# Kernel tuning notes

Hardware: AMD Instinct MI355X
Metric: run time of the kernel (lower is better)

Reference implementation:

```python
import jax, jax.numpy as jnp
import numpy as np

B, C, T, F = 2, 256, 1024, 64
N, HID = 4, 64


def setup_inputs() -> dict:
    key = jax.random.key(0)
    ks = jax.random.split(key, 9)
    s = 0.02
    return {
        "x": jax.random.normal(ks[0], (B, C, T, F), dtype=jnp.float32),
        "Wq": jax.random.normal(ks[1], (N, HID, C), dtype=jnp.float32) * s,
        "bq": jnp.zeros((N, HID), dtype=jnp.float32),
        "Wk": jax.random.normal(ks[2], (N, HID, C), dtype=jnp.float32) * s,
        "bk": jnp.zeros((N, HID), dtype=jnp.float32),
        "Wv": jax.random.normal(ks[3], (N, C // N, C), dtype=jnp.float32) * s,
        "bv": jnp.zeros((N, C // N), dtype=jnp.float32),
        "Wp": jax.random.normal(ks[4], (C, C), dtype=jnp.float32) * s,
        "bp": jnp.zeros((C,), dtype=jnp.float32),
    }


def reference(x, Wq, bq, Wk, bk, Wv, bv, Wp, bp):
    b, c, t, f = x.shape
    n = Wq.shape[0]
    # conv1x1 per head then torch: cat(dim=0) -> [N*b, h, t, f]; transpose(1,2); flatten -> [N*b, t, h*f]
    def proj(W, bias):
        h = W.shape[1]
        y = jnp.einsum('bctf,nhc->nbthf', x, W) + bias[:, None, None, :, None]
        return y.reshape(n * b, t, h * f)

    Q = proj(Wq, bq)                       # [N*b, t, hid*f]
    K = proj(Wk, bk)                       # [N*b, t, hid*f]
    V = proj(Wv, bv)                       # [N*b, t, (c/N)*f]

    scale = 1.0 / jnp.sqrt(jnp.asarray(Q.shape[-1], dtype=x.dtype))
    attn = jax.nn.softmax(jnp.einsum('mte,mse->mts', Q, K) * scale, axis=2)
    Vo = jnp.einsum('mts,msd->mtd', attn, V)             # [N*b, t, c*f/N]

    # torch: reshape(b*N, t, c*f//N).transpose(1,2).view(N,b,c//N,t,f).transpose(0,1).view(b,c,t,f)
    Vo = Vo.transpose(0, 2, 1)                            # [N*b, c*f/N, t]
    Vo = Vo.reshape(n, b, c // n, t, f)
    Vo = jnp.swapaxes(Vo, 0, 1).reshape(b, c, t, f)

    out = jnp.einsum('bctf,oc->botf', Vo, Wp) + bp[None, :, None, None]
    return out + x
```

## Files before the change

kernel.cpp:

```cpp
#include <hip/hip_runtime.h>

#define DI __device__ __forceinline__

static constexpr int B_ = 2;
static constexpr int C_ = 256;
static constexpr int T_ = 1024;
static constexpr int F_ = 64;
static constexpr int M_ = 8;
static constexpr int E_ = 4096;
static constexpr float SCALE_ = 1.0f / 64.0f;

typedef __attribute__((ext_vector_type(8))) short bf16x8;
typedef __attribute__((ext_vector_type(4))) float f32x4;

DI unsigned short bf16_rne(float f) {
    unsigned int u = __float_as_uint(f);
    return (unsigned short)((u + 0x7FFFu + ((u >> 16) & 1u)) >> 16);
}
DI float bf2f(unsigned short h) { return __uint_as_float(((unsigned int)h) << 16); }
DI ushort4 pack4(float a, float b, float c, float d) {
    return make_ushort4(bf16_rne(a), bf16_rne(b), bf16_rne(c), bf16_rne(d));
}
DI float4 up4(ushort4 u) {
    return make_float4(bf2f(u.x), bf2f(u.y), bf2f(u.z), bf2f(u.w));
}

DI void gload_lds16(const unsigned short* g, unsigned short* l) {
    __builtin_amdgcn_global_load_lds(
        (const __attribute__((address_space(1))) unsigned int*)g,
        (__attribute__((address_space(3))) unsigned int*)l, 16, 0, 0);
}

DI void mfma16(f32x4& acc, bf16x8 a, bf16x8 b) {
    asm("v_mfma_f32_16x16x32_bf16 %0, %1, %2, %0" : "+v"(acc) : "v"(a), "v"(b));
}

__global__ __launch_bounds__(256) void wconv_kernel(
    const float* __restrict__ Wq, const float* __restrict__ Wk,
    const float* __restrict__ Wv, const float* __restrict__ Wp,
    const float* __restrict__ bq, const float* __restrict__ bk,
    const float* __restrict__ bv,
    unsigned short* __restrict__ Wall, unsigned short* __restrict__ Wpb,
    float* __restrict__ bias_all)
{
    const int tid = (int)threadIdx.x;
    const int bid = (int)blockIdx.x;
    if (bid < 192) {
        const int idx = (bid * 256 + tid) * 4;
        const int proj = idx >> 16, rem = idx & 65535;
        const float* src = proj == 0 ? Wq : (proj == 1 ? Wk : Wv);
        float4 v = *(const float4*)(src + rem);
        *(ushort4*)(Wall + idx) = pack4(v.x, v.y, v.z, v.w);
        const int gid = bid * 256 + tid;
        if (gid < 768) {
            float bb = gid < 256 ? bq[gid] : (gid < 512 ? bk[gid - 256] : bv[gid - 512]);
            bias_all[gid] = bb;
        }
    } else {
        const int idx = ((bid - 192) * 256 + tid) * 4;
        float4 v = *(const float4*)(Wp + idx);
        *(ushort4*)(Wpb + idx) = pack4(v.x, v.y, v.z, v.w);
    }
}

__global__ __launch_bounds__(256) void qkv_one(
    const float* __restrict__ x, const unsigned short* __restrict__ Wall,
    const float* __restrict__ bias_all, unsigned short* __restrict__ outQ)
{
    const int wgid = (int)blockIdx.x;
    const int b = wgid >> 9, tft = wgid & 511;
    const int tfbase = tft * 128;

    const int tid = (int)threadIdx.x;
    const int wid = tid >> 6, lane = tid & 63;
    const int wr = wid >> 1, wc = wid & 1;
    const int lo16 = lane & 15, hi4 = lane >> 4;

    __shared__ unsigned short As[4 * 128 * 64];
    __shared__ unsigned short Bs[128 * 64];

    {
        const int a = lane & 7, cg = lane >> 3;
        const int rowb = wid * 32 + a * 4;
        const float* xb = x + (size_t)b * (C_ * T_ * F_) + tfbase + rowb;
        for (int cb = 0; cb < 256; cb += 64) {
            const int c0 = cb + cg * 8;
            float4 v[8];
#pragma unroll
            for (int g = 0; g < 8; ++g)
                v[g] = *(const float4*)(xb + (size_t)(c0 + g) * 65536);
            const int kc = cb >> 6;
#pragma unroll
            for (int j = 0; j < 4; ++j) {
                const int row = rowb + j;
                const int col8 = cg ^ (row & 7);
                ushort4 lo = pack4(v[0].x + 0.f, v[1].x, v[2].x, v[3].x);
                float e0 = (&v[0].x)[j], e1 = (&v[1].x)[j], e2 = (&v[2].x)[j], e3 = (&v[3].x)[j];
                float e4 = (&v[4].x)[j], e5 = (&v[5].x)[j], e6 = (&v[6].x)[j], e7 = (&v[7].x)[j];
                ushort4 p0 = pack4(e0, e1, e2, e3);
                ushort4 p1 = pack4(e4, e5, e6, e7);
                (void)lo;
                *(ushort4*)&As[kc * 8192 + row * 64 + col8 * 8]     = p0;
                *(ushort4*)&As[kc * 8192 + row * 64 + col8 * 8 + 4] = p1;
            }
        }
    }

    const int srow = lane >> 3;
    const int scol = ((lane & 7) ^ srow) * 8;
    const int tf0 = tfbase + wr * 64;

    __syncthreads();

    for (int ntl = 0; ntl < 6; ++ntl) {
        const int nbase = ntl * 128;
        const unsigned short* brow = Wall + (size_t)nbase * 256;
        f32x4 acc[4][4] = {};

        for (int kc = 0; kc < 4; ++kc) {
#pragma unroll
            for (int i = 0; i < 4; ++i) {
                const int rb = wid * 32 + i * 8;
                gload_lds16(brow + (size_t)(rb + srow) * 256 + kc * 64 + scol,
                            &Bs[rb * 64]);
            }
            __syncthreads();
#pragma unroll
            for (int kk = 0; kk < 2; ++kk) {
                const int hc = (kk * 32 + hi4 * 8) ^ ((lane & 7) << 3);
                bf16x8 a[4], bb[4];
#pragma unroll
                for (int mi = 0; mi < 4; ++mi)
                    a[mi] = *(const bf16x8*)&As[kc * 8192 + (wr * 64 + mi * 16 + lo16) * 64 + hc];
#pragma unroll
                for (int nj = 0; nj < 4; ++nj)
                    bb[nj] = *(const bf16x8*)&Bs[(wc * 64 + nj * 16 + lo16) * 64 + hc];
#pragma unroll
                for (int mi = 0; mi < 4; ++mi)
#pragma unroll
                    for (int nj = 0; nj < 4; ++nj)
                        mfma16(acc[mi][nj], a[mi], bb[nj]);
            }
            __syncthreads();
        }

        asm volatile("s_nop 7\n\ts_nop 7" ::: "memory");
#pragma unroll
        for (int nj = 0; nj < 4; ++nj) {
            const int r_col = nbase + wc * 64 + nj * 16 + lo16;
            const int projl = r_col >> 8;
            const int rr = r_col & 255;
            const int mrow = (rr >> 6) * 2 + b;
            const int h = rr & 63;
            const float bv = bias_all[r_col];
            unsigned short* dst0 = outQ + (size_t)projl * 33554432
                                 + (size_t)mrow * (T_ * E_) + h * 64;
#pragma unroll
            for (int mi = 0; mi < 4; ++mi) {
                const int tf = tf0 + mi * 16 + hi4 * 4;
                const int t = tf >> 6, f = tf & 63;
                *(ushort4*)(dst0 + (size_t)t * E_ + f) =
                    pack4(acc[mi][nj][0] + bv, acc[mi][nj][1] + bv,
                          acc[mi][nj][2] + bv, acc[mi][nj][3] + bv);
            }
        }
        if (ntl < 5) __syncthreads();
    }
}

__global__ __launch_bounds__(256) void scores_mfma(
    const unsigned short* __restrict__ Q, const unsigned short* __restrict__ K,
    unsigned short* __restrict__ S)
{
    const int orig = (int)blockIdx.x;
    const int wg = (orig & 7) * 64 + (orig >> 3);
    const int m = wg >> 6;
    const int rest = wg & 63;
    const int sbase = (rest & 7) * 128;
    const int tbase = (rest >> 3) * 128;
    const int tid = (int)threadIdx.x;
    const int wid = tid >> 6, lane = tid & 63;
    const int wr = wid >> 1, wc = wid & 1;
    const int lo16 = lane & 15, hi4 = lane >> 4;

    __shared__ unsigned short As[128 * 64];
    __shared__ unsigned short Bs[128 * 64];

    f32x4 acc[4][4] = {};

    const unsigned short* qrow = Q + ((size_t)m * T_ + tbase) * E_;
    const unsigned short* krow = K + ((size_t)m * T_ + sbase) * E_;

    const int srow = lane >> 3;
    const int scol = ((lane & 7) ^ srow) * 8;

    for (int eb = 0; eb < E_; eb += 64) {
#pragma unroll
        for (int i = 0; i < 4; ++i) {
            const int rb = wid * 32 + i * 8;
            gload_lds16(qrow + (size_t)(rb + srow) * E_ + eb + scol, &As[rb * 64]);
            gload_lds16(krow + (size_t)(rb + srow) * E_ + eb + scol, &Bs[rb * 64]);
        }
        __syncthreads();
#pragma unroll
        for (int kk = 0; kk < 2; ++kk) {
            const int hc = (kk * 32 + hi4 * 8) ^ ((lane & 7) << 3);
            bf16x8 a[4], bb[4];
#pragma unroll
            for (int mi = 0; mi < 4; ++mi)
                a[mi] = *(const bf16x8*)&As[(wr * 64 + mi * 16 + lo16) * 64 + hc];
#pragma unroll
            for (int nj = 0; nj < 4; ++nj)
                bb[nj] = *(const bf16x8*)&Bs[(wc * 64 + nj * 16 + lo16) * 64 + hc];
#pragma unroll
            for (int mi = 0; mi < 4; ++mi)
#pragma unroll
                for (int nj = 0; nj < 4; ++nj)
                    mfma16(acc[mi][nj], a[mi], bb[nj]);
        }
        __syncthreads();
    }

    asm volatile("s_nop 7\n\ts_nop 7" ::: "memory");
#pragma unroll
    for (int mi = 0; mi < 4; ++mi)
#pragma unroll
        for (int r = 0; r < 4; ++r) {
            int trow = tbase + wr * 64 + mi * 16 + hi4 * 4 + r;
            unsigned short* sp = S + ((size_t)m * T_ + trow) * T_ + sbase + wc * 64 + lo16;
#pragma unroll
            for (int nj = 0; nj < 4; ++nj)
                sp[nj * 16] = bf16_rne(acc[mi][nj][r] * SCALE_);
        }
}

__global__ __launch_bounds__(256) void softmax_kernel(
    const unsigned short* __restrict__ S, unsigned short* __restrict__ A)
{
    const size_t rowoff = ((size_t)blockIdx.y * T_ + blockIdx.x) * T_;
    const int tid = (int)threadIdx.x;
    const int wid = tid >> 6, lane = tid & 63;

    __shared__ float redmx[4];
    __shared__ float redsm[4];

    float4 v = up4(*(const ushort4*)(S + rowoff + tid * 4));
    float mx = fmaxf(fmaxf(v.x, v.y), fmaxf(v.z, v.w));
#pragma unroll
    for (int off = 32; off > 0; off >>= 1) mx = fmaxf(mx, __shfl_xor(mx, off));
    if (lane == 0) redmx[wid] = mx;
    __syncthreads();
    mx = fmaxf(fmaxf(redmx[0], redmx[1]), fmaxf(redmx[2], redmx[3]));

    float e0 = __expf(v.x - mx), e1 = __expf(v.y - mx);
    float e2 = __expf(v.z - mx), e3 = __expf(v.w - mx);
    float sm = (e0 + e1) + (e2 + e3);
#pragma unroll
    for (int off = 32; off > 0; off >>= 1) sm += __shfl_xor(sm, off);
    if (lane == 0) redsm[wid] = sm;
    __syncthreads();
    sm = (redsm[0] + redsm[1]) + (redsm[2] + redsm[3]);
    float inv = 1.0f / sm;
    *(ushort4*)(A + rowoff + tid * 4) = pack4(e0 * inv, e1 * inv, e2 * inv, e3 * inv);
}

__global__ __launch_bounds__(256) void vt_kernel(
    const unsigned short* __restrict__ V, unsigned short* __restrict__ Vt)
{
    const int m = blockIdx.z;
    const int d0 = blockIdx.x * 64;
    const int s0 = blockIdx.y * 64;
    const int tid = (int)threadIdx.x;
    __shared__ unsigned short ts[64][68];

    const unsigned short* vp = V + (size_t)m * T_ * E_;
#pragma unroll
    for (int it = 0; it < 4; ++it) {
        int idx = it * 256 + tid;
        int sl = idx >> 4, d4 = (idx & 15) * 4;
        *(ushort4*)&ts[sl][d4] = *(const ushort4*)&vp[(size_t)(s0 + sl) * E_ + d0 + d4];
    }
    __syncthreads();
    unsigned short* op = Vt + (size_t)m * E_ * T_;
    const int dl = tid >> 2, s16 = (tid & 3) * 16;
#pragma unroll
    for (int q = 0; q < 4; ++q) {
        int s4 = s16 + q * 4;
        ushort4 v = make_ushort4(ts[s4][dl], ts[s4+1][dl], ts[s4+2][dl], ts[s4+3][dl]);
        *(ushort4*)&op[(size_t)(d0 + dl) * T_ + s0 + s4] = v;
    }
}

__global__ __launch_bounds__(256) void pv_mfma(
    const unsigned short* __restrict__ A, const unsigned short* __restrict__ Vt,
    unsigned short* __restrict__ G)
{
    const int orig = (int)blockIdx.x;
    const int wg = (orig & 7) * 256 + (orig >> 3);
    const int m = wg >> 8;
    const int rest = wg & 255;
    const int dbase = (rest & 31) * 128;
    const int tbase = (rest >> 5) * 128;
    const int nh = m >> 1, b = m & 1;
    const int tid = (int)threadIdx.x;
    const int wid = tid >> 6, lane = tid & 63;
    const int wr = wid >> 1, wc = wid & 1;
    const int lo16 = lane & 15, hi4 = lane >> 4;

    __shared__ unsigned short As[128 * 64];
    __shared__ unsigned short Bs[128 * 64];

    f32x4 acc[4][4] = {};

    const unsigned short* arow = A  + ((size_t)m * T_ + tbase) * T_;
    const unsigned short* vrow = Vt + (size_t)m * E_ * T_ + (size_t)dbase * T_;

    const int srow = lane >> 3;
    const int scol = ((lane & 7) ^ srow) * 8;

    for (int sb = 0; sb < T_; sb += 64) {
#pragma unroll
        for (int i = 0; i < 4; ++i) {
            const int rb = wid * 32 + i * 8;
            gload_lds16(arow + (size_t)(rb + srow) * T_ + sb + scol, &As[rb * 64]);
            gload_lds16(vrow + (size_t)(rb + srow) * T_ + sb + scol, &Bs[rb * 64]);
        }
        __syncthreads();
#pragma unroll
        for (int kk = 0; kk < 2; ++kk) {
            const int hc = (kk * 32 + hi4 * 8) ^ ((lane & 7) << 3);
            bf16x8 a[4], bb[4];
#pragma unroll
            for (int mi = 0; mi < 4; ++mi)
                a[mi] = *(const bf16x8*)&As[(wr * 64 + mi * 16 + lo16) * 64 + hc];
#pragma unroll
            for (int nj = 0; nj < 4; ++nj)
                bb[nj] = *(const bf16x8*)&Bs[(wc * 64 + nj * 16 + lo16) * 64 + hc];
#pragma unroll
            for (int mi = 0; mi < 4; ++mi)
#pragma unroll
                for (int nj = 0; nj < 4; ++nj)
                    mfma16(acc[mi][nj], a[mi], bb[nj]);
        }
        __syncthreads();
    }

    asm volatile("s_nop 7\n\ts_nop 7" ::: "memory");
    const int cb   = nh * 64 + (dbase >> 6) + wc;
    const int t2lo = (tbase >> 6) + wr;
#pragma unroll
    for (int mi = 0; mi < 4; ++mi) {
        const int tl = mi * 16 + hi4 * 4;
#pragma unroll
        for (int nj = 0; nj < 4; ++nj) {
            const int d63 = nj * 16 + lo16;
            size_t addr = (((size_t)(b * 256 + cb)) * 1024 + d63 * 16 + t2lo) * 64 + tl;
            *(ushort4*)&G[addr] = pack4(acc[mi][nj][0], acc[mi][nj][1],
                                        acc[mi][nj][2], acc[mi][nj][3]);
        }
    }
}

__global__ __launch_bounds__(256) void gt_kernel(
    const unsigned short* __restrict__ G, unsigned short* __restrict__ GT)
{
    const int tf0 = blockIdx.x * 64;
    const int c0  = blockIdx.y * 64;
    const int b   = blockIdx.z;
    const int tid = (int)threadIdx.x;
    __shared__ unsigned short ts[64][68];

    const unsigned short* gb = G + (size_t)(b * 256 + c0) * 65536 + tf0;
#pragma unroll
    for (int it = 0; it < 4; ++it) {
        int idx = it * 256 + tid;
        int cl = idx >> 4, tf4 = (idx & 15) * 4;
        *(ushort4*)&ts[cl][tf4] = *(const ushort4*)(gb + (size_t)cl * 65536 + tf4);
    }
    __syncthreads();
    const int tfl = tid >> 2, c16 = (tid & 3) * 16;
    unsigned short* op = GT + ((size_t)b * 65536 + tf0 + tfl) * 256 + c0 + c16;
#pragma unroll
    for (int q = 0; q < 4; ++q) {
        int cl = c16 + q * 4;
        ushort4 v = make_ushort4(ts[cl][tfl], ts[cl+1][tfl], ts[cl+2][tfl], ts[cl+3][tfl]);
        *(ushort4*)(op + q * 4) = v;
    }
}

__global__ __launch_bounds__(256) void outproj_mfma(
    const unsigned short* __restrict__ GT, const unsigned short* __restrict__ Wpb,
    const float* __restrict__ bp, const float* __restrict__ x,
    float* __restrict__ out)
{
    const int tfbase = blockIdx.x * 128;
    const int obase  = blockIdx.y * 128;
    const int b      = blockIdx.z;
    const int tid = (int)threadIdx.x;
    const int wid = tid >> 6, lane = tid & 63;
    const int wr = wid >> 1, wc = wid & 1;
    const int lo16 = lane & 15, hi4 = lane >> 4;

    __shared__ unsigned short As[128 * 64];
    __shared__ unsigned short Bs[128 * 64];

    f32x4 acc[4][4] = {};

    const unsigned short* arow = GT + ((size_t)b * 65536 + tfbase) * 256;
    const unsigned short* brow = Wpb + (size_t)obase * 256;

    const int srow = lane >> 3;
    const int scol = ((lane & 7) ^ srow) * 8;

    for (int cb = 0; cb < 256; cb += 64) {
#pragma unroll
        for (int i = 0; i < 4; ++i) {
            const int rb = wid * 32 + i * 8;
            gload_lds16(arow + (size_t)(rb + srow) * 256 + cb + scol, &As[rb * 64]);
            gload_lds16(brow + (size_t)(rb + srow) * 256 + cb + scol, &Bs[rb * 64]);
        }
        __syncthreads();
#pragma unroll
        for (int kk = 0; kk < 2; ++kk) {
            const int hc = (kk * 32 + hi4 * 8) ^ ((lane & 7) << 3);
            bf16x8 a[4], bb[4];
#pragma unroll
            for (int mi = 0; mi < 4; ++mi)
                a[mi] = *(const bf16x8*)&As[(wr * 64 + mi * 16 + lo16) * 64 + hc];
#pragma unroll
            for (int nj = 0; nj < 4; ++nj)
                bb[nj] = *(const bf16x8*)&Bs[(wc * 64 + nj * 16 + lo16) * 64 + hc];
#pragma unroll
            for (int mi = 0; mi < 4; ++mi)
#pragma unroll
                for (int nj = 0; nj < 4; ++nj)
                    mfma16(acc[mi][nj], a[mi], bb[nj]);
        }
        __syncthreads();
    }

    asm volatile("s_nop 7\n\ts_nop 7" ::: "memory");
#pragma unroll
    for (int nj = 0; nj < 4; ++nj) {
        const int o = obase + wc * 64 + nj * 16 + lo16;
        const float bias = bp[o];
        const size_t rowb = ((size_t)(b * 256 + o)) * 65536;
#pragma unroll
        for (int mi = 0; mi < 4; ++mi) {
            const int tf = tfbase + wr * 64 + mi * 16 + hi4 * 4;
            float4 xv = *(const float4*)(x + rowb + tf);
            float4 r = make_float4(acc[mi][nj][0] + bias + xv.x,
                                   acc[mi][nj][1] + bias + xv.y,
                                   acc[mi][nj][2] + bias + xv.z,
                                   acc[mi][nj][3] + bias + xv.w);
            *(float4*)(out + rowb + tf) = r;
        }
    }
}

extern "C" void kernel_launch(void* const* d_in, const int* in_sizes, int n_in,
                              void* d_out, int out_size, void* d_ws, size_t ws_size,
                              hipStream_t stream) {
    const float* x  = (const float*)d_in[0];
    const float* Wq = (const float*)d_in[1];
    const float* bq = (const float*)d_in[2];
    const float* Wk = (const float*)d_in[3];
    const float* bk = (const float*)d_in[4];
    const float* Wv = (const float*)d_in[5];
    const float* bv = (const float*)d_in[6];
    const float* Wp = (const float*)d_in[7];
    const float* bp = (const float*)d_in[8];
    float* out = (float*)d_out;

    char* ws = (char*)d_ws;
    unsigned short* Q    = (unsigned short*)(ws);
    unsigned short* K    = (unsigned short*)(ws + 67108864);
    unsigned short* V    = (unsigned short*)(ws + 134217728);
    unsigned short* S    = (unsigned short*)(ws + 201326592);
    unsigned short* A    = (unsigned short*)(ws + 218103808);
    unsigned short* Wall = (unsigned short*)(ws + 234881024);
    float* bias_all      = (float*)(ws + 235274240);
    unsigned short* Wpb  = (unsigned short*)(ws + 235277312);
    unsigned short* Vt = K;
    unsigned short* G  = Q;
    unsigned short* GT = V;

    wconv_kernel<<<256, 256, 0, stream>>>(Wq, Wk, Wv, Wp, bq, bk, bv, Wall, Wpb, bias_all);
    qkv_one<<<1024, 256, 0, stream>>>(x, Wall, bias_all, Q);
    scores_mfma<<<512, 256, 0, stream>>>(Q, K, S);
    softmax_kernel<<<dim3(T_, M_), 256, 0, stream>>>(S, A);
    vt_kernel<<<dim3(64, 16, M_), 256, 0, stream>>>(V, Vt);
    pv_mfma<<<2048, 256, 0, stream>>>(A, Vt, G);
    gt_kernel<<<dim3(1024, 4, 2), 256, 0, stream>>>(G, GT);
    outproj_mfma<<<dim3(512, 2, 2), 256, 0, stream>>>(GT, Wpb, bp, x, out);
}
```

Baseline: 409.5 us.

## Halve QKV projection M-tile to 64 rows and prefetch x loads

Result: no change. 417.4 us (+1.9%).

```diff
diff --git a/kernel.cpp b/kernel.cpp
--- a/kernel.cpp
+++ b/kernel.cpp
@@ -63,59 +63,64 @@
     }
 }
 
-__global__ __launch_bounds__(256) void qkv_one(
+__global__ __launch_bounds__(256) void qkv_two(
     const float* __restrict__ x, const unsigned short* __restrict__ Wall,
     const float* __restrict__ bias_all, unsigned short* __restrict__ outQ)
 {
     const int wgid = (int)blockIdx.x;
-    const int b = wgid >> 9, tft = wgid & 511;
-    const int tfbase = tft * 128;
+    const int b = wgid >> 10, tft = wgid & 1023;
+    const int tfbase = tft * 64;
 
     const int tid = (int)threadIdx.x;
     const int wid = tid >> 6, lane = tid & 63;
     const int wr = wid >> 1, wc = wid & 1;
     const int lo16 = lane & 15, hi4 = lane >> 4;
 
-    __shared__ unsigned short As[4 * 128 * 64];
+    __shared__ unsigned short As[4 * 64 * 64];
     __shared__ unsigned short Bs[128 * 64];
 
     {
-        const int a = lane & 7, cg = lane >> 3;
-        const int rowb = wid * 32 + a * 4;
+        const int a = lane & 3, cg = lane >> 2;
+        const int rowb = wid * 16 + a * 4;
         const float* xb = x + (size_t)b * (C_ * T_ * F_) + tfbase + rowb;
-        for (int cb = 0; cb < 256; cb += 64) {
-            const int c0 = cb + cg * 8;
-            float4 v[8];
-#pragma unroll
-            for (int g = 0; g < 8; ++g)
-                v[g] = *(const float4*)(xb + (size_t)(c0 + g) * 65536);
-            const int kc = cb >> 6;
+        const size_t cstep = 65536;
+
+        float4 va[4], vb[4];
+#pragma unroll
+        for (int g = 0; g < 4; ++g)
+            va[g] = *(const float4*)(xb + (size_t)(cg * 4 + g) * cstep);
+
+#pragma unroll
+        for (int cb = 0; cb < 4; ++cb) {
+            if (cb < 3) {
+                const int c0n = (cb + 1) * 64 + cg * 4;
+#pragma unroll
+                for (int g = 0; g < 4; ++g)
+                    vb[g] = *(const float4*)(xb + (size_t)(c0n + g) * cstep);
+            }
 #pragma unroll
             for (int j = 0; j < 4; ++j) {
                 const int row = rowb + j;
-                const int col8 = cg ^ (row & 7);
-                ushort4 lo = pack4(v[0].x + 0.f, v[1].x, v[2].x, v[3].x);
-                float e0 = (&v[0].x)[j], e1 = (&v[1].x)[j], e2 = (&v[2].x)[j], e3 = (&v[3].x)[j];
-                float e4 = (&v[4].x)[j], e5 = (&v[5].x)[j], e6 = (&v[6].x)[j], e7 = (&v[7].x)[j];
-                ushort4 p0 = pack4(e0, e1, e2, e3);
-                ushort4 p1 = pack4(e4, e5, e6, e7);
-                (void)lo;
-                *(ushort4*)&As[kc * 8192 + row * 64 + col8 * 8]     = p0;
-                *(ushort4*)&As[kc * 8192 + row * 64 + col8 * 8 + 4] = p1;
+                const int phys = row * 64 + (((cg >> 1) ^ (row & 7)) << 3) + (cg & 1) * 4;
+                float e0 = (&va[0].x)[j], e1 = (&va[1].x)[j];
+                float e2 = (&va[2].x)[j], e3 = (&va[3].x)[j];
+                *(ushort4*)&As[cb * 4096 + phys] = pack4(e0, e1, e2, e3);
             }
+#pragma unroll
+            for (int g = 0; g < 4; ++g) va[g] = vb[g];
         }
     }
 
     const int srow = lane >> 3;
     const int scol = ((lane & 7) ^ srow) * 8;
-    const int tf0 = tfbase + wr * 64;
+    const int tf0 = tfbase + wr * 32;
 
     __syncthreads();
 
     for (int ntl = 0; ntl < 6; ++ntl) {
         const int nbase = ntl * 128;
         const unsigned short* brow = Wall + (size_t)nbase * 256;
-        f32x4 acc[4][4] = {};
+        f32x4 acc[2][4] = {};
 
         for (int kc = 0; kc < 4; ++kc) {
 #pragma unroll
@@ -128,15 +133,15 @@
 #pragma unroll
             for (int kk = 0; kk < 2; ++kk) {
                 const int hc = (kk * 32 + hi4 * 8) ^ ((lane & 7) << 3);
-                bf16x8 a[4], bb[4];
-#pragma unroll
-                for (int mi = 0; mi < 4; ++mi)
-                    a[mi] = *(const bf16x8*)&As[kc * 8192 + (wr * 64 + mi * 16 + lo16) * 64 + hc];
+                bf16x8 a[2], bb[4];
+#pragma unroll
+                for (int mi = 0; mi < 2; ++mi)
+                    a[mi] = *(const bf16x8*)&As[kc * 4096 + (wr * 32 + mi * 16 + lo16) * 64 + hc];
 #pragma unroll
                 for (int nj = 0; nj < 4; ++nj)
                     bb[nj] = *(const bf16x8*)&Bs[(wc * 64 + nj * 16 + lo16) * 64 + hc];
 #pragma unroll
-                for (int mi = 0; mi < 4; ++mi)
+                for (int mi = 0; mi < 2; ++mi)
 #pragma unroll
                     for (int nj = 0; nj < 4; ++nj)
                         mfma16(acc[mi][nj], a[mi], bb[nj]);
@@ -156,7 +161,7 @@
             unsigned short* dst0 = outQ + (size_t)projl * 33554432
                                  + (size_t)mrow * (T_ * E_) + h * 64;
 #pragma unroll
-            for (int mi = 0; mi < 4; ++mi) {
+            for (int mi = 0; mi < 2; ++mi) {
                 const int tf = tf0 + mi * 16 + hi4 * 4;
                 const int t = tf >> 6, f = tf & 63;
                 *(ushort4*)(dst0 + (size_t)t * E_ + f) =
@@ -164,7 +169,6 @@
                           acc[mi][nj][2] + bv, acc[mi][nj][3] + bv);
             }
         }
-        if (ntl < 5) __syncthreads();
     }
 }
 
@@ -486,7 +490,7 @@
     unsigned short* GT = V;
 
     wconv_kernel<<<256, 256, 0, stream>>>(Wq, Wk, Wv, Wp, bq, bk, bv, Wall, Wpb, bias_all);
-    qkv_one<<<1024, 256, 0, stream>>>(x, Wall, bias_all, Q);
+    qkv_two<<<2048, 256, 0, stream>>>(x, Wall, bias_all, Q);
     scores_mfma<<<512, 256, 0, stream>>>(Q, K, S);
     softmax_kernel<<<dim3(T_, M_), 256, 0, stream>>>(S, A);
     vt_kernel<<<dim3(64, 16, M_), 256, 0, stream>>>(V, Vt);
```
